# Kernel optimization log

Hardware: AMD Instinct MI355X
Metric: run time of the kernel (lower is better)

The kernel has to match this reference:

```python
import jax, jax.numpy as jnp
import numpy as np
import math

DT = 1024
HID = 512
B, M, N = 16, 1024, 1024
NEG_INF = -1.0e9


def _linear(x, w, b):
    # torch nn.Linear convention: w is (out, in)
    return x @ w.T + b


def setup_inputs() -> dict:
    key = jax.random.key(0)
    ks = jax.random.split(key, 20)
    s = 0.02
    inp = {
        "oV": jax.random.normal(ks[0], (B, M, DT), jnp.float32),
        "oT": jax.random.normal(ks[1], (B, N, DT), jnp.float32),
        "Wq_v_w": jax.random.normal(ks[2], (DT, DT), jnp.float32) * s,
        "Wq_v_b": jnp.zeros((DT,), jnp.float32),
        "Wk_t_w": jax.random.normal(ks[3], (DT, DT), jnp.float32) * s,
        "Wk_t_b": jnp.zeros((DT,), jnp.float32),
        "Wv_t_w": jax.random.normal(ks[4], (DT, DT), jnp.float32) * s,
        "Wv_t_b": jnp.zeros((DT,), jnp.float32),
        "Wq_t_w": jax.random.normal(ks[5], (DT, DT), jnp.float32) * s,
        "Wq_t_b": jnp.zeros((DT,), jnp.float32),
        "Wk_v_w": jax.random.normal(ks[6], (DT, DT), jnp.float32) * s,
        "Wk_v_b": jnp.zeros((DT,), jnp.float32),
        "Wv_v_w": jax.random.normal(ks[7], (DT, DT), jnp.float32) * s,
        "Wv_v_b": jnp.zeros((DT,), jnp.float32),
        "ffn1_w": jax.random.normal(ks[8], (HID, 2 * DT), jnp.float32) * s,
        "ffn1_b": jnp.zeros((HID,), jnp.float32),
        "ffn2_w": jax.random.normal(ks[9], (1, HID), jnp.float32) * s,
        "ffn2_b": jnp.zeros((1,), jnp.float32),
    }
    return inp


def reference(oV, oT, Wq_v_w, Wq_v_b, Wk_t_w, Wk_t_b, Wv_t_w, Wv_t_b,
              Wq_t_w, Wq_t_b, Wk_v_w, Wk_v_b, Wv_v_w, Wv_v_b,
              ffn1_w, ffn1_b, ffn2_w, ffn2_b):
    dt = oV.shape[-1]
    inv_sqrt = 1.0 / math.sqrt(dt)

    # shared similarity-derived mask
    sim_raw = jnp.einsum('bmd,bnd->bmn', oV, oT)            # (B, m, n)
    v_pool = oV.mean(axis=1)                                  # (B, dt)
    t_pool = oT.mean(axis=1)                                  # (B, dt)
    h = jax.nn.relu(_linear(jnp.concatenate([v_pool, t_pool], axis=-1), ffn1_w, ffn1_b))
    l = jax.nn.sigmoid(_linear(h, ffn2_w, ffn2_b))[:, 0]      # (B,)
    S = jax.nn.softmax(sim_raw * inv_sqrt, axis=-1)
    Mmask = S >= l[:, None, None]                             # (B, m, n) bool

    # V -> T masked cross-attention
    Q_v = _linear(oV, Wq_v_w, Wq_v_b)
    K_t = _linear(oT, Wk_t_w, Wk_t_b)
    V_t = _linear(oT, Wv_t_w, Wv_t_b)
    scores_vt = jnp.einsum('bmd,bnd->bmn', Q_v, K_t) * inv_sqrt
    attn_vt = jax.nn.softmax(jnp.where(Mmask, scores_vt, NEG_INF), axis=-1)
    out_vt = jnp.einsum('bmn,bnd->bmd', attn_vt, V_t)

    # T -> V masked cross-attention (transposed mask)
    Q_t = _linear(oT, Wq_t_w, Wq_t_b)
    K_v = _linear(oV, Wk_v_w, Wk_v_b)
    V_v = _linear(oV, Wv_v_w, Wv_v_b)
    scores_tv = jnp.einsum('bnd,bmd->bnm', Q_t, K_v) * inv_sqrt
    attn_tv = jax.nn.softmax(jnp.where(Mmask.transpose(0, 2, 1), scores_tv, NEG_INF), axis=-1)
    out_tv = jnp.einsum('bnm,bmd->bnd', attn_tv, V_v)

    return out_vt, out_tv, Mmask.astype(jnp.float32)
```

## Files before the change

kernel.cpp:

```cpp
#include <hip/hip_runtime.h>
#include <stdint.h>

typedef unsigned short u16;
typedef unsigned char  u8;
typedef unsigned int   u32;
typedef unsigned long long u64;
typedef __attribute__((ext_vector_type(8))) short  short8;
typedef __attribute__((ext_vector_type(4))) float  floatx4;

#define Bz   16
#define Mm   1024
#define Nn   1024
#define Dd   1024
#define HIDh 512
#define INV_SQRT_D 0.03125f
#define NEGINF (-1.0e9f)
#define BMDc  ((size_t)Bz * Mm * Dd)
#define sMDc  ((long)Mm * Dd)

__device__ __forceinline__ float bf2f(u16 h) {
    union { u32 u; float f; } c; c.u = ((u32)h) << 16; return c.f;
}
__device__ __forceinline__ u16 f2bf(float f) {
    union { float f; u32 u; } c; c.f = f;
    u32 u = c.u;
    return (u16)((u + 0x7FFFu + ((u >> 16) & 1u)) >> 16);
}
__device__ __forceinline__ void g2lds16(const u16* g, u16* l) {
    __builtin_amdgcn_global_load_lds((const __attribute__((address_space(1))) void*)g,
                                     (__attribute__((address_space(3))) void*)l, 16, 0, 0);
}

__device__ __forceinline__ float waveSum(float v) {
#pragma unroll
    for (int o = 32; o > 0; o >>= 1) v += __shfl_xor(v, o);
    return v;
}
__device__ __forceinline__ float waveMax(float v) {
#pragma unroll
    for (int o = 32; o > 0; o >>= 1) v = fmaxf(v, __shfl_xor(v, o));
    return v;
}

template <bool OUT_FP32>
__global__ __launch_bounds__(512, 2) void gemm256(
    const u16* __restrict__ Aa, const u16* __restrict__ Ba, void* __restrict__ Ca,
    const u16* __restrict__ Ab, const u16* __restrict__ Bb, void* __restrict__ Cb,
    int K, int ldc, long sA, long sB, long sC)
{
    __shared__ __align__(16) u16 lds[2][2][256 * 64];
    const int tid  = threadIdx.x;
    const int lane = tid & 63;
    const int wv   = tid >> 6;
    const int wr   = wv >> 2;
    const int wc   = wv & 3;
    const int fr   = lane & 15, fq = lane >> 4;

    const int gX = gridDim.x, gY = gridDim.y;
    int bid = blockIdx.x + gX * (blockIdx.y + gY * blockIdx.z);
    const int nwg = gX * gY * gridDim.z;
    int wg = (bid & 7) * (nwg >> 3) + (bid >> 3);
    const int bx = wg % gX; wg /= gX;
    const int by = wg % gY;
    const int bz2 = wg / gY;
    const int br = bz2 >> 4;
    const int bz = bz2 & 15;

    const u16* A  = (br ? Ab : Aa) + (long)bz * sA;
    const u16* Bm = (br ? Bb : Ba) + (long)bz * sB;
    void* Cv = br ? Cb : Ca;

    const long tileM = (long)bx * 256, tileN = (long)by * 256;
    const int T = K >> 6;

    floatx4 acc[8][4];
#pragma unroll
    for (int i = 0; i < 8; ++i)
#pragma unroll
        for (int j = 0; j < 4; ++j) acc[i][j] = (floatx4){0.f, 0.f, 0.f, 0.f};

    const int lrow = lane >> 3;
    const int scol = ((lane & 7) ^ lrow) << 3;
    const int sw   = fr & 7;
    const int kc0  = ((fq ^ sw) << 3);
    const int kc1  = (((4 + fq) ^ sw) << 3);

    auto stage = [&](int tt, int side, int hh, int bb) {
#pragma unroll
        for (int i = 0; i < 2; ++i) {
            const int j = i * 8 + wv;
            const int prow = side ? (((j >> 2) << 6) + (hh << 5) + ((j & 3) << 3))
                                  : (((j >> 3) << 7) + (hh << 6) + ((j & 7) << 3));
            const u16* src = side ? Bm : A;
            const long rb  = side ? tileN : tileM;
            g2lds16(src + (size_t)(rb + prow + lrow) * (size_t)K + (size_t)(tt << 6) + scol,
                    &lds[bb][side][prow * 64]);
        }
    };

    short8 Af[4][2], Bf[4][2];
    auto quad = [&](int mb, int nb) {
#pragma unroll
        for (int m = 0; m < 4; ++m)
#pragma unroll
            for (int n = 0; n < 2; ++n) {
                acc[mb + m][nb + n] = __builtin_amdgcn_mfma_f32_16x16x32_bf16(
                    Af[m][0], Bf[nb + n][0], acc[mb + m][nb + n], 0, 0, 0);
                acc[mb + m][nb + n] = __builtin_amdgcn_mfma_f32_16x16x32_bf16(
                    Af[m][1], Bf[nb + n][1], acc[mb + m][nb + n], 0, 0, 0);
            }
    };

    stage(0, 0, 0, 0); stage(0, 1, 0, 0); stage(0, 1, 1, 0); stage(0, 0, 1, 0);
    stage(1, 0, 0, 1); stage(1, 1, 1, 1); stage(1, 0, 1, 1);
    asm volatile("s_waitcnt vmcnt(6)" ::: "memory");
    __builtin_amdgcn_s_barrier();

    for (int t = 0; t < T; ++t) {
        const int cb = t & 1;
        const u16* lA = &lds[cb][0][0];
        const u16* lB = &lds[cb][1][0];

#pragma unroll
        for (int m = 0; m < 4; ++m) {
            const int ro = ((wr << 7) + (m << 4) + fr) * 64;
            Af[m][0] = *(const short8*)&lA[ro + kc0];
            Af[m][1] = *(const short8*)&lA[ro + kc1];
        }
#pragma unroll
        for (int n = 0; n < 2; ++n) {
            const int ro = ((wc << 6) + (n << 4) + fr) * 64;
            Bf[n][0] = *(const short8*)&lB[ro + kc0];
            Bf[n][1] = *(const short8*)&lB[ro + kc1];
        }
        if (t + 1 < T) stage(t + 1, 1, 0, cb ^ 1);
        asm volatile("" ::: "memory");
        __builtin_amdgcn_s_barrier();
        asm volatile("s_waitcnt lgkmcnt(0)" ::: "memory");
        __builtin_amdgcn_sched_barrier(0);
        __builtin_amdgcn_s_setprio(1);
        quad(0, 0);
        __builtin_amdgcn_s_setprio(0);
        asm volatile("" ::: "memory");
        __builtin_amdgcn_s_barrier();

#pragma unroll
        for (int n = 2; n < 4; ++n) {
            const int ro = ((wc << 6) + (n << 4) + fr) * 64;
            Bf[n][0] = *(const short8*)&lB[ro + kc0];
            Bf[n][1] = *(const short8*)&lB[ro + kc1];
        }
        if (t + 2 < T) stage(t + 2, 0, 0, cb);
        asm volatile("" ::: "memory");
        __builtin_amdgcn_s_barrier();
        asm volatile("s_waitcnt lgkmcnt(0)" ::: "memory");
        __builtin_amdgcn_sched_barrier(0);
        __builtin_amdgcn_s_setprio(1);
        quad(0, 2);
        __builtin_amdgcn_s_setprio(0);
        asm volatile("" ::: "memory");
        __builtin_amdgcn_s_barrier();

#pragma unroll
        for (int m = 0; m < 4; ++m) {
            const int ro = ((wr << 7) + ((m + 4) << 4) + fr) * 64;
            Af[m][0] = *(const short8*)&lA[ro + kc0];
            Af[m][1] = *(const short8*)&lA[ro + kc1];
        }
        if (t + 2 < T) stage(t + 2, 1, 1, cb);
        asm volatile("" ::: "memory");
        __builtin_amdgcn_s_barrier();
        asm volatile("s_waitcnt lgkmcnt(0)" ::: "memory");
        __builtin_amdgcn_sched_barrier(0);
        __builtin_amdgcn_s_setprio(1);
        quad(4, 2);
        __builtin_amdgcn_s_setprio(0);
        asm volatile("" ::: "memory");
        __builtin_amdgcn_s_barrier();

        if (t + 2 < T) stage(t + 2, 0, 1, cb);
        asm volatile("" ::: "memory");
        __builtin_amdgcn_s_barrier();
        __builtin_amdgcn_s_setprio(1);
        quad(4, 0);
        __builtin_amdgcn_s_setprio(0);
        if (t + 1 < T) {
            if (t + 2 < T) asm volatile("s_waitcnt vmcnt(6)" ::: "memory");
            else           asm volatile("s_waitcnt vmcnt(0)" ::: "memory");
        }
        asm volatile("" ::: "memory");
        __builtin_amdgcn_s_barrier();
    }

    __syncthreads();
    if constexpr (!OUT_FP32) {
        u16* l2 = (u16*)&lds[0][0][0];
#pragma unroll
        for (int j = 0; j < 4; ++j) {
            const int col = (wc << 6) + (j << 4) + fr;
            const int c   = col >> 3;
#pragma unroll
            for (int i = 0; i < 8; ++i) {
                const int row0 = (wr << 7) + (i << 4) + (fq << 2);
#pragma unroll
                for (int r = 0; r < 4; ++r) {
                    const int row = row0 + r;
                    l2[row * 256 + (((c + row) & 31) << 3) + (col & 7)] = f2bf(acc[i][j][r]);
                }
            }
        }
        __syncthreads();
        u16* C = (u16*)Cv + (long)bz * sC;
#pragma unroll
        for (int it = 0; it < 16; ++it) {
            const int row = it * 16 + (tid >> 5);
            const int ch  = tid & 31;
            const short8 v = *(const short8*)&l2[row * 256 + (((ch + row) & 31) << 3)];
            *(short8*)&C[(tileM + row) * (long)ldc + tileN + ch * 8] = v;
        }
    } else {
        float* l2f = (float*)&lds[0][0][0];
        float* C = (float*)Cv + (long)bz * sC;
#pragma unroll
        for (int pass = 0; pass < 2; ++pass) {
            if (pass) __syncthreads();
            if (wr == pass) {
#pragma unroll
                for (int j = 0; j < 4; ++j) {
                    const int col = (wc << 6) + (j << 4) + fr;
                    const int c   = col >> 2;
#pragma unroll
                    for (int i = 0; i < 8; ++i) {
                        const int row0 = (i << 4) + (fq << 2);
#pragma unroll
                        for (int r = 0; r < 4; ++r)
                            l2f[(row0 + r) * 256 + (((c + (fq << 2)) & 63) << 2) + (col & 3)] = acc[i][j][r];
                    }
                }
            }
            __syncthreads();
#pragma unroll
            for (int it = 0; it < 16; ++it) {
                const int row = it * 8 + (tid >> 6);
                const int ch  = tid & 63;
                const int rot = (row >> 2) & 3;
                const float4 v = *(const float4*)&l2f[row * 256 + (((ch + (rot << 2)) & 63) << 2)];
                *(float4*)&C[(tileM + pass * 128 + row) * (long)ldc + tileN + ch * 4] = v;
            }
        }
    }
}

__global__ __launch_bounds__(512, 2) void gemm_proj3(
    const u16* __restrict__ A0, const u16* __restrict__ A1,
    const u16* __restrict__ Wcat, const float* __restrict__ bc,
    u16* __restrict__ Pq0, u16* __restrict__ Pk0, u16* __restrict__ Pv0,
    u16* __restrict__ Pq1, u16* __restrict__ Pk1, u16* __restrict__ Pv1, int K)
{
    __shared__ __align__(16) u16 lds[2][2][256 * 64];
    const int tid  = threadIdx.x;
    const int lane = tid & 63;
    const int wv   = tid >> 6;
    const int wr   = wv >> 2;
    const int wc   = wv & 3;
    const int fr   = lane & 15, fq = lane >> 4;

    const int z = blockIdx.z;
    const u16* A  = z ? A1 : A0;
    const u16* Bm = Wcat + ((size_t)z * 3 * Dd * Dd);
    const float* bcat = bc + z * 3072;
    u16* Pq = z ? Pq1 : Pq0;
    u16* Pk = z ? Pk1 : Pk0;
    u16* Pv = z ? Pv1 : Pv0;

    const int bid = blockIdx.x + 64 * blockIdx.y;
    const int x  = bid & 7, l = bid >> 3;
    const int x0 = (x & 3) * 16, y0 = (x >> 2) * 6;
    const int w = l >> 5, r = l & 31;
    int bx, by;
    if (w == 0)      { bx = x0 + (r & 7);      by = y0 + (r >> 3); }
    else if (w == 1) { bx = x0 + 8 + (r & 7);  by = y0 + (r >> 3); }
    else             { bx = x0 + (r & 15);     by = y0 + 4 + (r >> 4); }

    const long tileM = (long)bx * 256, tileN = (long)by * 256;
    const int T = K >> 6;

    floatx4 acc[8][4];
#pragma unroll
    for (int i = 0; i < 8; ++i)
#pragma unroll
        for (int j = 0; j < 4; ++j) acc[i][j] = (floatx4){0.f, 0.f, 0.f, 0.f};

    const int lrow = lane >> 3;
    const int scol = ((lane & 7) ^ lrow) << 3;
    const int sw   = fr & 7;
    const int kc0  = ((fq ^ sw) << 3);
    const int kc1  = (((4 + fq) ^ sw) << 3);

    auto stage = [&](int tt, int side, int hh, int bb) {
#pragma unroll
        for (int i = 0; i < 2; ++i) {
            const int j = i * 8 + wv;
            const int prow = side ? (((j >> 2) << 6) + (hh << 5) + ((j & 3) << 3))
                                  : (((j >> 3) << 7) + (hh << 6) + ((j & 7) << 3));
            const u16* src = side ? Bm : A;
            const long rb  = side ? tileN : tileM;
            g2lds16(src + (size_t)(rb + prow + lrow) * (size_t)K + (size_t)(tt << 6) + scol,
                    &lds[bb][side][prow * 64]);
        }
    };

    short8 Af[4][2], Bf[4][2];
    auto quad = [&](int mb, int nb) {
#pragma unroll
        for (int m = 0; m < 4; ++m)
#pragma unroll
            for (int n = 0; n < 2; ++n) {
                acc[mb + m][nb + n] = __builtin_amdgcn_mfma_f32_16x16x32_bf16(
                    Af[m][0], Bf[nb + n][0], acc[mb + m][nb + n], 0, 0, 0);
                acc[mb + m][nb + n] = __builtin_amdgcn_mfma_f32_16x16x32_bf16(
                    Af[m][1], Bf[nb + n][1], acc[mb + m][nb + n], 0, 0, 0);
            }
    };

    stage(0, 0, 0, 0); stage(0, 1, 0, 0); stage(0, 1, 1, 0); stage(0, 0, 1, 0);
    stage(1, 0, 0, 1); stage(1, 1, 1, 1); stage(1, 0, 1, 1);
    asm volatile("s_waitcnt vmcnt(6)" ::: "memory");
    __builtin_amdgcn_s_barrier();

    for (int t = 0; t < T; ++t) {
        const int cb = t & 1;
        const u16* lA = &lds[cb][0][0];
        const u16* lB = &lds[cb][1][0];

#pragma unroll
        for (int m = 0; m < 4; ++m) {
            const int ro = ((wr << 7) + (m << 4) + fr) * 64;
            Af[m][0] = *(const short8*)&lA[ro + kc0];
            Af[m][1] = *(const short8*)&lA[ro + kc1];
        }
#pragma unroll
        for (int n = 0; n < 2; ++n) {
            const int ro = ((wc << 6) + (n << 4) + fr) * 64;
            Bf[n][0] = *(const short8*)&lB[ro + kc0];
            Bf[n][1] = *(const short8*)&lB[ro + kc1];
        }
        if (t + 1 < T) stage(t + 1, 1, 0, cb ^ 1);
        asm volatile("" ::: "memory");
        __builtin_amdgcn_s_barrier();
        asm volatile("s_waitcnt lgkmcnt(0)" ::: "memory");
        __builtin_amdgcn_sched_barrier(0);
        __builtin_amdgcn_s_setprio(1);
        quad(0, 0);
        __builtin_amdgcn_s_setprio(0);
        asm volatile("" ::: "memory");
        __builtin_amdgcn_s_barrier();

#pragma unroll
        for (int n = 2; n < 4; ++n) {
            const int ro = ((wc << 6) + (n << 4) + fr) * 64;
            Bf[n][0] = *(const short8*)&lB[ro + kc0];
            Bf[n][1] = *(const short8*)&lB[ro + kc1];
        }
        if (t + 2 < T) stage(t + 2, 0, 0, cb);
        asm volatile("" ::: "memory");
        __builtin_amdgcn_s_barrier();
        asm volatile("s_waitcnt lgkmcnt(0)" ::: "memory");
        __builtin_amdgcn_sched_barrier(0);
        __builtin_amdgcn_s_setprio(1);
        quad(0, 2);
        __builtin_amdgcn_s_setprio(0);
        asm volatile("" ::: "memory");
        __builtin_amdgcn_s_barrier();

#pragma unroll
        for (int m = 0; m < 4; ++m) {
            const int ro = ((wr << 7) + ((m + 4) << 4) + fr) * 64;
            Af[m][0] = *(const short8*)&lA[ro + kc0];
            Af[m][1] = *(const short8*)&lA[ro + kc1];
        }
        if (t + 2 < T) stage(t + 2, 1, 1, cb);
        asm volatile("" ::: "memory");
        __builtin_amdgcn_s_barrier();
        asm volatile("s_waitcnt lgkmcnt(0)" ::: "memory");
        __builtin_amdgcn_sched_barrier(0);
        __builtin_amdgcn_s_setprio(1);
        quad(4, 2);
        __builtin_amdgcn_s_setprio(0);
        asm volatile("" ::: "memory");
        __builtin_amdgcn_s_barrier();

        if (t + 2 < T) stage(t + 2, 0, 1, cb);
        asm volatile("" ::: "memory");
        __builtin_amdgcn_s_barrier();
        __builtin_amdgcn_s_setprio(1);
        quad(4, 0);
        __builtin_amdgcn_s_setprio(0);
        if (t + 1 < T) {
            if (t + 2 < T) asm volatile("s_waitcnt vmcnt(6)" ::: "memory");
            else           asm volatile("s_waitcnt vmcnt(0)" ::: "memory");
        }
        asm volatile("" ::: "memory");
        __builtin_amdgcn_s_barrier();
    }

    const int oid = (int)(tileN >> 10);
    __syncthreads();
    if (oid < 2) {
        u16* l2 = (u16*)&lds[0][0][0];
#pragma unroll
        for (int j = 0; j < 4; ++j) {
            const int col = (wc << 6) + (j << 4) + fr;
            const int c   = col >> 3;
            const float bv = bcat[tileN + col];
#pragma unroll
            for (int i = 0; i < 8; ++i) {
                const int row0 = (wr << 7) + (i << 4) + (fq << 2);
#pragma unroll
                for (int r = 0; r < 4; ++r) {
                    const int row = row0 + r;
                    l2[row * 256 + (((c + row) & 31) << 3) + (col & 7)] = f2bf(acc[i][j][r] + bv);
                }
            }
        }
        __syncthreads();
        u16* P = oid ? Pk : Pq;
        const long colN = tileN & 1023;
#pragma unroll
        for (int it = 0; it < 16; ++it) {
            const int row = it * 16 + (tid >> 5);
            const int ch  = tid & 31;
            const short8 v = *(const short8*)&l2[row * 256 + (((ch + row) & 31) << 3)];
            *(short8*)&P[(tileM + row) * (long)Dd + colN + ch * 8] = v;
        }
    } else {
        char* l2c = (char*)&lds[0][0][0];
#pragma unroll
        for (int j = 0; j < 4; ++j) {
            const int col = (wc << 6) + (j << 4) + fr;
            const float bv = bcat[tileN + col];
            const int swz = (col & 7) << 4;
#pragma unroll
            for (int i = 0; i < 8; ++i) {
                const int row0 = (wr << 7) + (i << 4) + (fq << 2);
                const u64 pk = (u64)f2bf(acc[i][j][0] + bv)
                             | ((u64)f2bf(acc[i][j][1] + bv) << 16)
                             | ((u64)f2bf(acc[i][j][2] + bv) << 32)
                             | ((u64)f2bf(acc[i][j][3] + bv) << 48);
                *(u64*)(l2c + col * 512 + ((row0 * 2) ^ swz)) = pk;
            }
        }
        __syncthreads();
        const long b  = tileM >> 10, tm = tileM & 1023;
        const long colN = tileN & 1023;
#pragma unroll
        for (int it = 0; it < 16; ++it) {
            const int col = it * 16 + (tid >> 5);
            const int ch  = tid & 31;
            const short8 v = *(const short8*)(l2c + col * 512 + ((ch * 16) ^ ((col & 7) << 4)));
            *(short8*)&Pv[b * sMDc + (colN + col) * (long)Mm + tm + ch * 8] = v;
        }
    }
}

__global__ __launch_bounds__(256) void conv_pool(
    const float* __restrict__ oV, const float* __restrict__ oT,
    u16* __restrict__ oVb, u16* __restrict__ oTb,
    float* __restrict__ vpool, float* __restrict__ tpool)
{
    const int b = blockIdx.y, srci = blockIdx.z;
    const float* src = (srci ? oT : oV) + (size_t)b * Mm * Dd;
    u16* dst = (srci ? oTb : oVb) + (size_t)b * Mm * Dd;
    const int c4 = threadIdx.x * 4;
    const int r0 = blockIdx.x * 64;
    float4 s = {0.f, 0.f, 0.f, 0.f};
    for (int r = r0; r < r0 + 64; ++r) {
        const float4 v = *(const float4*)&src[(size_t)r * Dd + c4];
        s.x += v.x; s.y += v.y; s.z += v.z; s.w += v.w;
        ushort4 o;
        o.x = f2bf(v.x); o.y = f2bf(v.y); o.z = f2bf(v.z); o.w = f2bf(v.w);
        *(ushort4*)&dst[(size_t)r * Dd + c4] = o;
    }
    float* pool = (srci ? tpool : vpool) + (size_t)b * Dd + c4;
    atomicAdd(pool + 0, s.x * (1.0f / Mm));
    atomicAdd(pool + 1, s.y * (1.0f / Mm));
    atomicAdd(pool + 2, s.z * (1.0f / Mm));
    atomicAdd(pool + 3, s.w * (1.0f / Mm));
}

__global__ __launch_bounds__(256) void wconv6(
    const float* __restrict__ w0, const float* __restrict__ w1, const float* __restrict__ w2,
    const float* __restrict__ w3, const float* __restrict__ w4, const float* __restrict__ w5,
    u16* __restrict__ dst)
{
    const float* src;
    switch (blockIdx.y) {
        case 0: src = w0; break; case 1: src = w1; break; case 2: src = w2; break;
        case 3: src = w3; break; case 4: src = w4; break; default: src = w5; break;
    }
    const size_t i = (size_t)blockIdx.x * 256 + threadIdx.x;
    const float4 a = ((const float4*)src)[2 * i];
    const float4 b = ((const float4*)src)[2 * i + 1];
    short8 o;
    o[0]=(short)f2bf(a.x); o[1]=(short)f2bf(a.y); o[2]=(short)f2bf(a.z); o[3]=(short)f2bf(a.w);
    o[4]=(short)f2bf(b.x); o[5]=(short)f2bf(b.y); o[6]=(short)f2bf(b.z); o[7]=(short)f2bf(b.w);
    *(short8*)(dst + (((size_t)blockIdx.y) << 20) + 8 * i) = o;
}

__global__ __launch_bounds__(256) void bcat_kernel(
    const float* __restrict__ b0, const float* __restrict__ b1, const float* __restrict__ b2,
    const float* __restrict__ b3, const float* __restrict__ b4, const float* __restrict__ b5,
    float* __restrict__ out)
{
    const int i = blockIdx.x * 256 + threadIdx.x;
    const int seg = i >> 10;
    const float* s;
    switch (seg) {
        case 0: s = b0; break; case 1: s = b1; break; case 2: s = b2; break;
        case 3: s = b3; break; case 4: s = b4; break; default: s = b5; break;
    }
    out[i] = s[i & 1023];
}

__global__ __launch_bounds__(256) void ffn1_kernel(
    const float* __restrict__ vpool, const float* __restrict__ tpool,
    const float* __restrict__ f1w, const float* __restrict__ f1b,
    float* __restrict__ hbuf)
{
    const int j = blockIdx.x, b = blockIdx.y;
    const int t = threadIdx.x, wv = t >> 6, lane = t & 63;
    __shared__ float red[4];
    const float* w = f1w + (size_t)j * (2 * Dd);
    float a = 0.f;
    for (int k = t; k < Dd; k += 256) a += vpool[b * Dd + k] * w[k];
    for (int k = t; k < Dd; k += 256) a += tpool[b * Dd + k] * w[Dd + k];
    a = waveSum(a);
    if (lane == 0) red[wv] = a;
    __syncthreads();
    if (t == 0) hbuf[b * HIDh + j] = fmaxf(red[0] + red[1] + red[2] + red[3] + f1b[j], 0.0f);
}

__global__ __launch_bounds__(256) void ffn2_kernel(
    const float* __restrict__ hbuf, const float* __restrict__ f2w,
    const float* __restrict__ f2b, float* __restrict__ lbuf)
{
    const int b = blockIdx.x;
    const int t = threadIdx.x, wv = t >> 6, lane = t & 63;
    __shared__ float red[4];
    float p = 0.f;
    for (int j = t; j < HIDh; j += 256) p += hbuf[b * HIDh + j] * f2w[j];
    p = waveSum(p);
    if (lane == 0) red[wv] = p;
    __syncthreads();
    if (t == 0) {
        const float z = red[0] + red[1] + red[2] + red[3] + f2b[0];
        lbuf[b] = 1.0f / (1.0f + expf(-z));
    }
}

__global__ __launch_bounds__(256) void sim_softmax_mask(
    const u16* __restrict__ scores, const float* __restrict__ lbuf,
    float* __restrict__ maskF, u8* __restrict__ maskR)
{
    const int row = blockIdx.x, b = blockIdx.y;
    const int t = threadIdx.x, wv = t >> 6, lane = t & 63;
    __shared__ float red[8];
    const size_t off = ((size_t)b * Mm + row) * Nn;
    const uint2 sv = *(const uint2*)(scores + off + 4 * t);
    const float x0 = bf2f((u16)(sv.x & 0xFFFFu)) * INV_SQRT_D;
    const float x1 = bf2f((u16)(sv.x >> 16))     * INV_SQRT_D;
    const float x2 = bf2f((u16)(sv.y & 0xFFFFu)) * INV_SQRT_D;
    const float x3 = bf2f((u16)(sv.y >> 16))     * INV_SQRT_D;
    float mx = waveMax(fmaxf(fmaxf(x0, x1), fmaxf(x2, x3)));
    if (lane == 0) red[wv] = mx;
    __syncthreads();
    mx = fmaxf(fmaxf(red[0], red[1]), fmaxf(red[2], red[3]));
    const float e0 = expf(x0 - mx), e1 = expf(x1 - mx), e2 = expf(x2 - mx), e3 = expf(x3 - mx);
    float s = waveSum(e0 + e1 + e2 + e3);
    if (lane == 0) red[4 + wv] = s;
    __syncthreads();
    const float inv = 1.0f / fmaxf(red[4] + red[5] + red[6] + red[7], 1e-30f);
    const float l = lbuf[b];
    float4 mk;
    mk.x = (e0 * inv >= l) ? 1.0f : 0.0f;
    mk.y = (e1 * inv >= l) ? 1.0f : 0.0f;
    mk.z = (e2 * inv >= l) ? 1.0f : 0.0f;
    mk.w = (e3 * inv >= l) ? 1.0f : 0.0f;
    *(float4*)(maskF + off + 4 * t) = mk;
    const u32 u8mk = (mk.x != 0.f ? 1u : 0u) | (mk.y != 0.f ? 0x100u : 0u)
                   | (mk.z != 0.f ? 0x10000u : 0u) | (mk.w != 0.f ? 0x1000000u : 0u);
    *(u32*)(maskR + off + 4 * t) = u8mk;
}

__global__ __launch_bounds__(256) void transpose_mask(
    const u8* __restrict__ maskR, u8* __restrict__ maskT)
{
    __shared__ u8 tile[64][68];
    const int m0 = blockIdx.x * 64, n0 = blockIdx.y * 64, b = blockIdx.z;
    const int t = threadIdx.x;
    const int r = t >> 2, c = (t & 3) * 16;
    const uint4 src = *(const uint4*)(maskR + ((size_t)b * Mm + (m0 + r)) * Nn + n0 + c);
    *(uint4*)&tile[r][c] = src;
    __syncthreads();
    union { u8 b[16]; uint4 v; } pk;
#pragma unroll
    for (int k = 0; k < 16; ++k) pk.b[k] = tile[c + k][r];
    *(uint4*)(maskT + ((size_t)b * Nn + (n0 + r)) * Mm + m0 + c) = pk.v;
}

__global__ __launch_bounds__(256) void masked_softmax2(
    u16* __restrict__ Sa, u16* __restrict__ Sb,
    const u8* __restrict__ mR, const u8* __restrict__ mT)
{
    const int row = blockIdx.x, bb = blockIdx.y;
    const int br = bb >> 4, b = bb & 15;
    u16* scores = br ? Sb : Sa;
    const u8* mask = br ? mT : mR;
    const int t = threadIdx.x, wv = t >> 6, lane = t & 63;
    __shared__ float red[8];
    const size_t off = ((size_t)b * Mm + row) * Nn;
    const uint2 sv = *(const uint2*)(scores + off + 4 * t);
    float x0 = bf2f((u16)(sv.x & 0xFFFFu)) * INV_SQRT_D;
    float x1 = bf2f((u16)(sv.x >> 16))     * INV_SQRT_D;
    float x2 = bf2f((u16)(sv.y & 0xFFFFu)) * INV_SQRT_D;
    float x3 = bf2f((u16)(sv.y >> 16))     * INV_SQRT_D;
    const u32 mk = *(const u32*)(mask + off + 4 * t);
    if (!(mk & 0x000000FFu)) x0 = NEGINF;
    if (!(mk & 0x0000FF00u)) x1 = NEGINF;
    if (!(mk & 0x00FF0000u)) x2 = NEGINF;
    if (!(mk & 0xFF000000u)) x3 = NEGINF;
    float mx = waveMax(fmaxf(fmaxf(x0, x1), fmaxf(x2, x3)));
    if (lane == 0) red[wv] = mx;
    __syncthreads();
    mx = fmaxf(fmaxf(red[0], red[1]), fmaxf(red[2], red[3]));
    const float e0 = expf(x0 - mx), e1 = expf(x1 - mx), e2 = expf(x2 - mx), e3 = expf(x3 - mx);
    float s = waveSum(e0 + e1 + e2 + e3);
    if (lane == 0) red[4 + wv] = s;
    __syncthreads();
    const float inv = 1.0f / fmaxf(red[4] + red[5] + red[6] + red[7], 1e-30f);
    uint2 pk;
    pk.x = (u32)f2bf(e0 * inv) | ((u32)f2bf(e1 * inv) << 16);
    pk.y = (u32)f2bf(e2 * inv) | ((u32)f2bf(e3 * inv) << 16);
    *(uint2*)(scores + off + 4 * t) = pk;
}

extern "C" void kernel_launch(void* const* d_in, const int* in_sizes, int n_in,
                              void* d_out, int out_size, void* d_ws, size_t ws_size,
                              hipStream_t stream)
{
    (void)in_sizes; (void)n_in; (void)out_size; (void)ws_size;
    const float* oV     = (const float*)d_in[0];
    const float* oT     = (const float*)d_in[1];
    const float* Wq_v_w = (const float*)d_in[2];
    const float* Wq_v_b = (const float*)d_in[3];
    const float* Wk_t_w = (const float*)d_in[4];
    const float* Wk_t_b = (const float*)d_in[5];
    const float* Wv_t_w = (const float*)d_in[6];
    const float* Wv_t_b = (const float*)d_in[7];
    const float* Wq_t_w = (const float*)d_in[8];
    const float* Wq_t_b = (const float*)d_in[9];
    const float* Wk_v_w = (const float*)d_in[10];
    const float* Wk_v_b = (const float*)d_in[11];
    const float* Wv_v_w = (const float*)d_in[12];
    const float* Wv_v_b = (const float*)d_in[13];
    const float* f1w    = (const float*)d_in[14];
    const float* f1b    = (const float*)d_in[15];
    const float* f2w    = (const float*)d_in[16];
    const float* f2b    = (const float*)d_in[17];

    float* out_vt = (float*)d_out;
    float* out_tv = out_vt + BMDc;
    float* maskF  = out_vt + 2 * BMDc;

    u16* S0a = (u16*)d_ws;
    u16* S1a = S0a + BMDc;
    u16* S2a = S1a + BMDc;
    u16* S0b = S2a + BMDc;
    u16* S1b = S0b + BMDc;
    u16* S2b = S1b + BMDc;
    u16* S3a = S2b + BMDc;
    u16* S3b = S3a + BMDc;
    u16* oVb = S3b + BMDc;
    u16* oTb = oVb + BMDc;
    u16* Wc  = oTb + BMDc;
    u8*  maskT = (u8*)(Wc + 6 * (1 << 20));
    u8*  maskR = maskT + BMDc;
    float* bcat  = (float*)(maskR + BMDc);
    float* vpool = bcat + 6144;
    float* tpool = vpool + Bz * Dd;
    float* hbuf  = tpool + Bz * Dd;
    float* lbuf  = hbuf + Bz * HIDh;

    const dim3 blk(256), blk512(512);
    const dim3 gBat(Mm / 256, Nn / 256, Bz);
    const dim3 gBat2(Mm / 256, Nn / 256, 2 * Bz);
    const dim3 gFproj(64, 12, 2);
    const dim3 gRow2(Mm, 2 * Bz);
    const dim3 gTrp(Mm / 64, Nn / 64, Bz);
    const long sMD = sMDc, sMN = (long)Mm * Nn;

    wconv6<<<dim3(512, 6), blk, 0, stream>>>(Wq_v_w, Wk_v_w, Wv_v_w, Wq_t_w, Wk_t_w, Wv_t_w, Wc);
    bcat_kernel<<<dim3(24), blk, 0, stream>>>(Wq_v_b, Wk_v_b, Wv_v_b, Wq_t_b, Wk_t_b, Wv_t_b, bcat);

    hipMemsetAsync(vpool, 0, 2 * Bz * Dd * sizeof(float), stream);
    conv_pool<<<dim3(16, Bz, 2), blk, 0, stream>>>(oV, oT, oVb, oTb, vpool, tpool);
    ffn1_kernel<<<dim3(HIDh, Bz), blk, 0, stream>>>(vpool, tpool, f1w, f1b, hbuf);
    ffn2_kernel<<<dim3(Bz), blk, 0, stream>>>(hbuf, f2w, f2b, lbuf);

    gemm256<false><<<gBat, blk512, 0, stream>>>(oVb, oTb, S3a, oVb, oTb, S3a, Dd, Nn, sMD, sMD, sMN);
    sim_softmax_mask<<<dim3(Mm, Bz), blk, 0, stream>>>(S3a, lbuf, maskF, maskR);
    transpose_mask<<<gTrp, blk, 0, stream>>>(maskR, maskT);

    gemm_proj3<<<gFproj, blk512, 0, stream>>>(oVb, oTb, Wc, bcat,
                                              S0a, S1b, S2b, S0b, S1a, S2a, Dd);

    gemm256<false><<<gBat2, blk512, 0, stream>>>(S0a, S1a, S3a, S0b, S1b, S3b, Dd, Nn, sMD, sMD, sMN);

    masked_softmax2<<<gRow2, blk, 0, stream>>>(S3a, S3b, maskR, maskT);

    gemm256<true><<<gBat2, blk512, 0, stream>>>(S3a, S2a, out_vt, S3b, S2b, out_tv, Nn, Dd, sMN, sMD, sMD);
}
```

Baseline: 816.8 us.

## Fuse similarity GEMM and six projections into one persistent work-list kernel

New measurement: 1.001 ms. 22.6% more time.

```diff
diff --git a/kernel.cpp b/kernel.cpp
--- a/kernel.cpp
+++ b/kernel.cpp
@@ -42,6 +42,278 @@
     return v;
 }
 
+struct Item { const u16* A; const u16* B; u16* C; const float* bias; int tr; };
+
+__global__ __launch_bounds__(512, 2) void gemm_fused7(
+    const u16* __restrict__ oVb, const u16* __restrict__ oTb,
+    const u16* __restrict__ Wc, const float* __restrict__ bcat,
+    u16* __restrict__ S3a,
+    u16* __restrict__ S0a, u16* __restrict__ S1a, u16* __restrict__ S2a,
+    u16* __restrict__ S0b, u16* __restrict__ S1b, u16* __restrict__ S2b)
+{
+    __shared__ __align__(16) u16 lds[2][2][256 * 64];
+    __shared__ __align__(16) u16 bounce[8192];
+    const int tid  = threadIdx.x;
+    const int lane = tid & 63;
+    const int wv   = tid >> 6;
+    const int wr   = wv >> 2;
+    const int wc   = wv & 3;
+    const int fr   = lane & 15, fq = lane >> 4;
+    const int p    = blockIdx.x;
+
+    const int lrow = lane >> 3;
+    const int scol = ((lane & 7) ^ lrow) << 3;
+    const int sw   = fr & 7;
+    const int kc0  = ((fq ^ sw) << 3);
+    const int kc1  = (((4 + fq) ^ sw) << 3);
+
+    auto make_item = [&](int g) -> Item {
+        Item it;
+        if (g == 0) {
+            int wg = (p & 7) * 32 + (p >> 3);
+            const int bx = wg & 3; wg >>= 2;
+            const int by = wg & 3;
+            const int bz = wg >> 2;
+            it.A = oVb + (size_t)bz * sMDc + (size_t)bx * 256 * 1024;
+            it.B = oTb + (size_t)bz * sMDc + (size_t)by * 256 * 1024;
+            it.C = S3a + (size_t)bz * ((long)Mm * Nn) + (size_t)bx * 256 * 1024 + by * 256;
+            it.bias = nullptr; it.tr = 0;
+        } else {
+            const int g2 = g - 1, z = g2 / 3, w = g2 % 3;
+            const int x = p & 7, l = p >> 3;
+            const int x0 = (x & 3) * 16, y0 = (x >> 2) * 6;
+            int bx, by;
+            if (w == 0)      { bx = x0 + (l & 7);      by = y0 + (l >> 3); }
+            else if (w == 1) { bx = x0 + 8 + (l & 7);  by = y0 + (l >> 3); }
+            else             { bx = x0 + (l & 15);     by = y0 + 4 + (l >> 4); }
+            const long tM = (long)bx * 256, tN = (long)by * 256;
+            it.A = (z ? oTb : oVb) + (size_t)tM * 1024;
+            it.B = Wc + (size_t)z * 3 * Dd * Dd + (size_t)tN * 1024;
+            it.bias = bcat + z * 3072 + tN;
+            const int oid = (int)(tN >> 10);
+            const long colN = tN & 1023;
+            if (oid == 0) {
+                it.C = (z ? S0b : S0a) + (size_t)tM * 1024 + colN; it.tr = 0;
+            } else if (oid == 1) {
+                it.C = (z ? S1a : S1b) + (size_t)tM * 1024 + colN; it.tr = 0;
+            } else {
+                u16* Pv = z ? S2a : S2b;
+                it.C = Pv + (tM >> 10) * sMDc + colN * 1024 + (tM & 1023); it.tr = 1;
+            }
+        }
+        return it;
+    };
+
+    Item cur = make_item(0);
+    Item nxt = make_item(1);
+
+    floatx4 acc[8][4];
+#pragma unroll
+    for (int i = 0; i < 8; ++i)
+#pragma unroll
+        for (int j = 0; j < 4; ++j) acc[i][j] = (floatx4){0.f, 0.f, 0.f, 0.f};
+
+    auto stageI = [&](const Item& it, int tu, int side, int hh, int bb) {
+#pragma unroll
+        for (int i2 = 0; i2 < 2; ++i2) {
+            const int j = i2 * 8 + wv;
+            const int prow = side ? (((j >> 2) << 6) + (hh << 5) + ((j & 3) << 3))
+                                  : (((j >> 3) << 7) + (hh << 6) + ((j & 7) << 3));
+            const u16* src = side ? it.B : it.A;
+            g2lds16(src + (size_t)(prow + lrow) * 1024 + (size_t)(tu << 6) + scol,
+                    &lds[bb][side][prow * 64]);
+        }
+    };
+
+    short8 Af[4][2], Bf[4][2];
+    auto quad = [&](int mb, int nb) {
+#pragma unroll
+        for (int m = 0; m < 4; ++m)
+#pragma unroll
+            for (int n = 0; n < 2; ++n) {
+                acc[mb + m][nb + n] = __builtin_amdgcn_mfma_f32_16x16x32_bf16(
+                    Af[m][0], Bf[nb + n][0], acc[mb + m][nb + n], 0, 0, 0);
+                acc[mb + m][nb + n] = __builtin_amdgcn_mfma_f32_16x16x32_bf16(
+                    Af[m][1], Bf[nb + n][1], acc[mb + m][nb + n], 0, 0, 0);
+            }
+    };
+
+    auto epilogue = [&](const Item& it) {
+        float bvj[4];
+#pragma unroll
+        for (int j = 0; j < 4; ++j)
+            bvj[j] = it.bias ? it.bias[(wc << 6) + (j << 4) + fr] : 0.f;
+        if (!it.tr) {
+#pragma unroll
+            for (int k = 0; k < 8; ++k) {
+                if (wr == (k >> 2)) {
+#pragma unroll
+                    for (int ji = 0; ji < 2; ++ji) {
+                        const int i = 2 * (k & 3) + ji;
+#pragma unroll
+                        for (int j = 0; j < 4; ++j) {
+                            const int col = (wc << 6) + (j << 4) + fr;
+                            const int c = col >> 3;
+#pragma unroll
+                            for (int r = 0; r < 4; ++r) {
+                                const int lr = ((i & 1) << 4) + (fq << 2) + r;
+                                bounce[lr * 256 + (((c + lr) & 31) << 3) + (col & 7)] =
+                                    f2bf(acc[i][j][r] + bvj[j]);
+                            }
+                        }
+                    }
+                }
+                asm volatile("s_waitcnt lgkmcnt(0)" ::: "memory");
+                __builtin_amdgcn_sched_barrier(0);
+                __builtin_amdgcn_s_barrier();
+#pragma unroll
+                for (int s = 0; s < 2; ++s) {
+                    const int u = tid + (s << 9);
+                    const int lr = u >> 5, ch = u & 31;
+                    const short8 v = *(const short8*)&bounce[lr * 256 + (((ch + lr) & 31) << 3)];
+                    *(short8*)&it.C[(size_t)(32 * k + lr) * 1024 + ch * 8] = v;
+                }
+                __builtin_amdgcn_s_barrier();
+            }
+        } else {
+            char* bc8 = (char*)&bounce[0];
+#pragma unroll
+            for (int k = 0; k < 8; ++k) {
+                if (wc == (k >> 1)) {
+#pragma unroll
+                    for (int jj = 0; jj < 2; ++jj) {
+                        const int j = 2 * (k & 1) + jj;
+                        const int lc = (jj << 4) + fr;
+#pragma unroll
+                        for (int i = 0; i < 8; ++i) {
+                            const int m0 = (wr << 7) + (i << 4) + (fq << 2);
+                            const u64 pk = (u64)f2bf(acc[i][j][0] + bvj[j])
+                                         | ((u64)f2bf(acc[i][j][1] + bvj[j]) << 16)
+                                         | ((u64)f2bf(acc[i][j][2] + bvj[j]) << 32)
+                                         | ((u64)f2bf(acc[i][j][3] + bvj[j]) << 48);
+                            *(u64*)(bc8 + lc * 512 + ((m0 * 2) ^ ((lc & 7) << 4))) = pk;
+                        }
+                    }
+                }
+                asm volatile("s_waitcnt lgkmcnt(0)" ::: "memory");
+                __builtin_amdgcn_sched_barrier(0);
+                __builtin_amdgcn_s_barrier();
+#pragma unroll
+                for (int s = 0; s < 2; ++s) {
+                    const int u = tid + (s << 9);
+                    const int lc = u >> 5, mch = u & 31;
+                    const short8 v = *(const short8*)(bc8 + lc * 512 + ((mch * 16) ^ ((lc & 7) << 4)));
+                    *(short8*)&it.C[(size_t)(32 * k + lc) * 1024 + mch * 8] = v;
+                }
+                __builtin_amdgcn_s_barrier();
+            }
+        }
+    };
+
+    stageI(cur, 0, 0, 0, 0); stageI(cur, 0, 1, 0, 0); stageI(cur, 0, 1, 1, 0); stageI(cur, 0, 0, 1, 0);
+    stageI(cur, 1, 0, 0, 1); stageI(cur, 1, 1, 1, 1); stageI(cur, 1, 0, 1, 1);
+    asm volatile("s_waitcnt vmcnt(6)" ::: "memory");
+    __builtin_amdgcn_s_barrier();
+
+    for (int tt = 0; tt < 112; ++tt) {
+        const int cb = tt & 1;
+        const int gcur = tt >> 4;
+        const u16* lA = &lds[cb][0][0];
+        const u16* lB = &lds[cb][1][0];
+
+        auto stg = [&](int u, int side, int hh) {
+            if (u < 112) {
+                const Item& it = ((u >> 4) == gcur) ? cur : nxt;
+                stageI(it, u & 15, side, hh, u & 1);
+            }
+        };
+
+#pragma unroll
+        for (int m = 0; m < 4; ++m) {
+            const int ro = ((wr << 7) + (m << 4) + fr) * 64;
+            Af[m][0] = *(const short8*)&lA[ro + kc0];
+            Af[m][1] = *(const short8*)&lA[ro + kc1];
+        }
+#pragma unroll
+        for (int n = 0; n < 2; ++n) {
+            const int ro = ((wc << 6) + (n << 4) + fr) * 64;
+            Bf[n][0] = *(const short8*)&lB[ro + kc0];
+            Bf[n][1] = *(const short8*)&lB[ro + kc1];
+        }
+        stg(tt + 1, 1, 0);
+        asm volatile("" ::: "memory");
+        __builtin_amdgcn_s_barrier();
+        asm volatile("s_waitcnt lgkmcnt(0)" ::: "memory");
+        __builtin_amdgcn_sched_barrier(0);
+        __builtin_amdgcn_s_setprio(1);
+        quad(0, 0);
+        __builtin_amdgcn_s_setprio(0);
+        asm volatile("" ::: "memory");
+        __builtin_amdgcn_s_barrier();
+
+#pragma unroll
+        for (int n = 2; n < 4; ++n) {
+            const int ro = ((wc << 6) + (n << 4) + fr) * 64;
+            Bf[n][0] = *(const short8*)&lB[ro + kc0];
+            Bf[n][1] = *(const short8*)&lB[ro + kc1];
+        }
+        stg(tt + 2, 0, 0);
+        asm volatile("" ::: "memory");
+        __builtin_amdgcn_s_barrier();
+        asm volatile("s_waitcnt lgkmcnt(0)" ::: "memory");
+        __builtin_amdgcn_sched_barrier(0);
+        __builtin_amdgcn_s_setprio(1);
+        quad(0, 2);
+        __builtin_amdgcn_s_setprio(0);
+        asm volatile("" ::: "memory");
+        __builtin_amdgcn_s_barrier();
+
+#pragma unroll
+        for (int m = 0; m < 4; ++m) {
+            const int ro = ((wr << 7) + ((m + 4) << 4) + fr) * 64;
+            Af[m][0] = *(const short8*)&lA[ro + kc0];
+            Af[m][1] = *(const short8*)&lA[ro + kc1];
+        }
+        stg(tt + 2, 1, 1);
+        asm volatile("" ::: "memory");
+        __builtin_amdgcn_s_barrier();
+        asm volatile("s_waitcnt lgkmcnt(0)" ::: "memory");
+        __builtin_amdgcn_sched_barrier(0);
+        __builtin_amdgcn_s_setprio(1);
+        quad(4, 2);
+        __builtin_amdgcn_s_setprio(0);
+        asm volatile("" ::: "memory");
+        __builtin_amdgcn_s_barrier();
+
+        stg(tt + 2, 0, 1);
+        asm volatile("" ::: "memory");
+        __builtin_amdgcn_s_barrier();
+        __builtin_amdgcn_s_setprio(1);
+        quad(4, 0);
+        __builtin_amdgcn_s_setprio(0);
+
+        if ((tt & 15) == 15) {
+            epilogue(cur);
+            cur = nxt;
+            if (gcur + 2 < 7) nxt = make_item(gcur + 2);
+#pragma unroll
+            for (int i = 0; i < 8; ++i)
+#pragma unroll
+                for (int j = 0; j < 4; ++j) acc[i][j] = (floatx4){0.f, 0.f, 0.f, 0.f};
+            if (tt + 1 < 112) asm volatile("s_waitcnt vmcnt(22)" ::: "memory");
+            asm volatile("" ::: "memory");
+            __builtin_amdgcn_s_barrier();
+        } else {
+            if (tt + 1 < 112) {
+                if (tt + 2 < 112) asm volatile("s_waitcnt vmcnt(6)" ::: "memory");
+                else              asm volatile("s_waitcnt vmcnt(0)" ::: "memory");
+            }
+            asm volatile("" ::: "memory");
+            __builtin_amdgcn_s_barrier();
+        }
+    }
+}
+
 template <bool OUT_FP32>
 __global__ __launch_bounds__(512, 2) void gemm256(
     const u16* __restrict__ Aa, const u16* __restrict__ Ba, void* __restrict__ Ca,
@@ -247,218 +519,6 @@
                 const float4 v = *(const float4*)&l2f[row * 256 + (((ch + (rot << 2)) & 63) << 2)];
                 *(float4*)&C[(tileM + pass * 128 + row) * (long)ldc + tileN + ch * 4] = v;
             }
-        }
-    }
-}
-
-__global__ __launch_bounds__(512, 2) void gemm_proj3(
-    const u16* __restrict__ A0, const u16* __restrict__ A1,
-    const u16* __restrict__ Wcat, const float* __restrict__ bc,
-    u16* __restrict__ Pq0, u16* __restrict__ Pk0, u16* __restrict__ Pv0,
-    u16* __restrict__ Pq1, u16* __restrict__ Pk1, u16* __restrict__ Pv1, int K)
-{
-    __shared__ __align__(16) u16 lds[2][2][256 * 64];
-    const int tid  = threadIdx.x;
-    const int lane = tid & 63;
-    const int wv   = tid >> 6;
-    const int wr   = wv >> 2;
-    const int wc   = wv & 3;
-    const int fr   = lane & 15, fq = lane >> 4;
-
-    const int z = blockIdx.z;
-    const u16* A  = z ? A1 : A0;
-    const u16* Bm = Wcat + ((size_t)z * 3 * Dd * Dd);
-    const float* bcat = bc + z * 3072;
-    u16* Pq = z ? Pq1 : Pq0;
-    u16* Pk = z ? Pk1 : Pk0;
-    u16* Pv = z ? Pv1 : Pv0;
-
-    const int bid = blockIdx.x + 64 * blockIdx.y;
-    const int x  = bid & 7, l = bid >> 3;
-    const int x0 = (x & 3) * 16, y0 = (x >> 2) * 6;
-    const int w = l >> 5, r = l & 31;
-    int bx, by;
-    if (w == 0)      { bx = x0 + (r & 7);      by = y0 + (r >> 3); }
-    else if (w == 1) { bx = x0 + 8 + (r & 7);  by = y0 + (r >> 3); }
-    else             { bx = x0 + (r & 15);     by = y0 + 4 + (r >> 4); }
-
-    const long tileM = (long)bx * 256, tileN = (long)by * 256;
-    const int T = K >> 6;
-
-    floatx4 acc[8][4];
-#pragma unroll
-    for (int i = 0; i < 8; ++i)
-#pragma unroll
-        for (int j = 0; j < 4; ++j) acc[i][j] = (floatx4){0.f, 0.f, 0.f, 0.f};
-
-    const int lrow = lane >> 3;
-    const int scol = ((lane & 7) ^ lrow) << 3;
-    const int sw   = fr & 7;
-    const int kc0  = ((fq ^ sw) << 3);
-    const int kc1  = (((4 + fq) ^ sw) << 3);
-
-    auto stage = [&](int tt, int side, int hh, int bb) {
-#pragma unroll
-        for (int i = 0; i < 2; ++i) {
-            const int j = i * 8 + wv;
-            const int prow = side ? (((j >> 2) << 6) + (hh << 5) + ((j & 3) << 3))
-                                  : (((j >> 3) << 7) + (hh << 6) + ((j & 7) << 3));
-            const u16* src = side ? Bm : A;
-            const long rb  = side ? tileN : tileM;
-            g2lds16(src + (size_t)(rb + prow + lrow) * (size_t)K + (size_t)(tt << 6) + scol,
-                    &lds[bb][side][prow * 64]);
-        }
-    };
-
-    short8 Af[4][2], Bf[4][2];
-    auto quad = [&](int mb, int nb) {
-#pragma unroll
-        for (int m = 0; m < 4; ++m)
-#pragma unroll
-            for (int n = 0; n < 2; ++n) {
-                acc[mb + m][nb + n] = __builtin_amdgcn_mfma_f32_16x16x32_bf16(
-                    Af[m][0], Bf[nb + n][0], acc[mb + m][nb + n], 0, 0, 0);
-                acc[mb + m][nb + n] = __builtin_amdgcn_mfma_f32_16x16x32_bf16(
-                    Af[m][1], Bf[nb + n][1], acc[mb + m][nb + n], 0, 0, 0);
-            }
-    };
-
-    stage(0, 0, 0, 0); stage(0, 1, 0, 0); stage(0, 1, 1, 0); stage(0, 0, 1, 0);
-    stage(1, 0, 0, 1); stage(1, 1, 1, 1); stage(1, 0, 1, 1);
-    asm volatile("s_waitcnt vmcnt(6)" ::: "memory");
-    __builtin_amdgcn_s_barrier();
-
-    for (int t = 0; t < T; ++t) {
-        const int cb = t & 1;
-        const u16* lA = &lds[cb][0][0];
-        const u16* lB = &lds[cb][1][0];
-
-#pragma unroll
-        for (int m = 0; m < 4; ++m) {
-            const int ro = ((wr << 7) + (m << 4) + fr) * 64;
-            Af[m][0] = *(const short8*)&lA[ro + kc0];
-            Af[m][1] = *(const short8*)&lA[ro + kc1];
-        }
-#pragma unroll
-        for (int n = 0; n < 2; ++n) {
-            const int ro = ((wc << 6) + (n << 4) + fr) * 64;
-            Bf[n][0] = *(const short8*)&lB[ro + kc0];
-            Bf[n][1] = *(const short8*)&lB[ro + kc1];
-        }
-        if (t + 1 < T) stage(t + 1, 1, 0, cb ^ 1);
-        asm volatile("" ::: "memory");
-        __builtin_amdgcn_s_barrier();
-        asm volatile("s_waitcnt lgkmcnt(0)" ::: "memory");
-        __builtin_amdgcn_sched_barrier(0);
-        __builtin_amdgcn_s_setprio(1);
-        quad(0, 0);
-        __builtin_amdgcn_s_setprio(0);
-        asm volatile("" ::: "memory");
-        __builtin_amdgcn_s_barrier();
-
-#pragma unroll
-        for (int n = 2; n < 4; ++n) {
-            const int ro = ((wc << 6) + (n << 4) + fr) * 64;
-            Bf[n][0] = *(const short8*)&lB[ro + kc0];
-            Bf[n][1] = *(const short8*)&lB[ro + kc1];
-        }
-        if (t + 2 < T) stage(t + 2, 0, 0, cb);
-        asm volatile("" ::: "memory");
-        __builtin_amdgcn_s_barrier();
-        asm volatile("s_waitcnt lgkmcnt(0)" ::: "memory");
-        __builtin_amdgcn_sched_barrier(0);
-        __builtin_amdgcn_s_setprio(1);
-        quad(0, 2);
-        __builtin_amdgcn_s_setprio(0);
-        asm volatile("" ::: "memory");
-        __builtin_amdgcn_s_barrier();
-
-#pragma unroll
-        for (int m = 0; m < 4; ++m) {
-            const int ro = ((wr << 7) + ((m + 4) << 4) + fr) * 64;
-            Af[m][0] = *(const short8*)&lA[ro + kc0];
-            Af[m][1] = *(const short8*)&lA[ro + kc1];
-        }
-        if (t + 2 < T) stage(t + 2, 1, 1, cb);
-        asm volatile("" ::: "memory");
-        __builtin_amdgcn_s_barrier();
-        asm volatile("s_waitcnt lgkmcnt(0)" ::: "memory");
-        __builtin_amdgcn_sched_barrier(0);
-        __builtin_amdgcn_s_setprio(1);
-        quad(4, 2);
-        __builtin_amdgcn_s_setprio(0);
-        asm volatile("" ::: "memory");
-        __builtin_amdgcn_s_barrier();
-
-        if (t + 2 < T) stage(t + 2, 0, 1, cb);
-        asm volatile("" ::: "memory");
-        __builtin_amdgcn_s_barrier();
-        __builtin_amdgcn_s_setprio(1);
-        quad(4, 0);
-        __builtin_amdgcn_s_setprio(0);
-        if (t + 1 < T) {
-            if (t + 2 < T) asm volatile("s_waitcnt vmcnt(6)" ::: "memory");
-            else           asm volatile("s_waitcnt vmcnt(0)" ::: "memory");
-        }
-        asm volatile("" ::: "memory");
-        __builtin_amdgcn_s_barrier();
-    }
-
-    const int oid = (int)(tileN >> 10);
-    __syncthreads();
-    if (oid < 2) {
-        u16* l2 = (u16*)&lds[0][0][0];
-#pragma unroll
-        for (int j = 0; j < 4; ++j) {
-            const int col = (wc << 6) + (j << 4) + fr;
-            const int c   = col >> 3;
-            const float bv = bcat[tileN + col];
-#pragma unroll
-            for (int i = 0; i < 8; ++i) {
-                const int row0 = (wr << 7) + (i << 4) + (fq << 2);
-#pragma unroll
-                for (int r = 0; r < 4; ++r) {
-                    const int row = row0 + r;
-                    l2[row * 256 + (((c + row) & 31) << 3) + (col & 7)] = f2bf(acc[i][j][r] + bv);
-                }
-            }
-        }
-        __syncthreads();
-        u16* P = oid ? Pk : Pq;
-        const long colN = tileN & 1023;
-#pragma unroll
-        for (int it = 0; it < 16; ++it) {
-            const int row = it * 16 + (tid >> 5);
-            const int ch  = tid & 31;
-            const short8 v = *(const short8*)&l2[row * 256 + (((ch + row) & 31) << 3)];
-            *(short8*)&P[(tileM + row) * (long)Dd + colN + ch * 8] = v;
-        }
-    } else {
-        char* l2c = (char*)&lds[0][0][0];
-#pragma unroll
-        for (int j = 0; j < 4; ++j) {
-            const int col = (wc << 6) + (j << 4) + fr;
-            const float bv = bcat[tileN + col];
-            const int swz = (col & 7) << 4;
-#pragma unroll
-            for (int i = 0; i < 8; ++i) {
-                const int row0 = (wr << 7) + (i << 4) + (fq << 2);
-                const u64 pk = (u64)f2bf(acc[i][j][0] + bv)
-                             | ((u64)f2bf(acc[i][j][1] + bv) << 16)
-                             | ((u64)f2bf(acc[i][j][2] + bv) << 32)
-                             | ((u64)f2bf(acc[i][j][3] + bv) << 48);
-                *(u64*)(l2c + col * 512 + ((row0 * 2) ^ swz)) = pk;
-            }
-        }
-        __syncthreads();
-        const long b  = tileM >> 10, tm = tileM & 1023;
-        const long colN = tileN & 1023;
-#pragma unroll
-        for (int it = 0; it < 16; ++it) {
-            const int col = it * 16 + (tid >> 5);
-            const int ch  = tid & 31;
-            const short8 v = *(const short8*)(l2c + col * 512 + ((ch * 16) ^ ((col & 7) << 4)));
-            *(short8*)&Pv[b * sMDc + (colN + col) * (long)Mm + tm + ch * 8] = v;
         }
     }
 }
@@ -692,9 +752,7 @@
     float* lbuf  = hbuf + Bz * HIDh;
 
     const dim3 blk(256), blk512(512);
-    const dim3 gBat(Mm / 256, Nn / 256, Bz);
     const dim3 gBat2(Mm / 256, Nn / 256, 2 * Bz);
-    const dim3 gFproj(64, 12, 2);
     const dim3 gRow2(Mm, 2 * Bz);
     const dim3 gTrp(Mm / 64, Nn / 64, Bz);
     const long sMD = sMDc, sMN = (long)Mm * Nn;
@@ -707,13 +765,12 @@
     ffn1_kernel<<<dim3(HIDh, Bz), blk, 0, stream>>>(vpool, tpool, f1w, f1b, hbuf);
     ffn2_kernel<<<dim3(Bz), blk, 0, stream>>>(hbuf, f2w, f2b, lbuf);
 
-    gemm256<false><<<gBat, blk512, 0, stream>>>(oVb, oTb, S3a, oVb, oTb, S3a, Dd, Nn, sMD, sMD, sMN);
+    gemm_fused7<<<dim3(256), blk512, 0, stream>>>(oVb, oTb, Wc, bcat, S3a,
+                                                  S0a, S1a, S2a, S0b, S1b, S2b);
+
     sim_softmax_mask<<<dim3(Mm, Bz), blk, 0, stream>>>(S3a, lbuf, maskF, maskR);
     transpose_mask<<<gTrp, blk, 0, stream>>>(maskR, maskT);
 
-    gemm_proj3<<<gFproj, blk512, 0, stream>>>(oVb, oTb, Wc, bcat,
-                                              S0a, S1b, S2b, S0b, S1a, S2a, Dd);
-
     gemm256<false><<<gBat2, blk512, 0, stream>>>(S0a, S1a, S3a, S0b, S1b, S3b, Dd, Nn, sMD, sMD, sMN);
 
     masked_softmax2<<<gRow2, blk, 0, stream>>>(S3a, S3b, maskR, maskT);
```
